# Kernel optimization log

Hardware: AMD Instinct MI355X
Metric: run time of the kernel (lower is better)

The kernel has to match this reference:

```python
import jax, jax.numpy as jnp
import numpy as np

DIM = 1024
NUM_HEADS = 16
HEAD_DIM = DIM // NUM_HEADS
SCALE = HEAD_DIM ** -0.5


def setup_inputs() -> dict:
    key = jax.random.key(0)
    k1, k2, k3 = jax.random.split(key, 3)
    x = jax.random.normal(k1, (4, 2048, DIM), dtype=jnp.float32)
    w_qkv = jax.random.normal(k2, (DIM, 3 * DIM), dtype=jnp.float32) * (DIM ** -0.5)
    b_qkv = jnp.zeros((3 * DIM,), dtype=jnp.float32)
    w_proj = jax.random.normal(k3, (DIM, DIM), dtype=jnp.float32) * (DIM ** -0.5)
    b_proj = jnp.zeros((DIM,), dtype=jnp.float32)
    return {"x": x, "w_qkv": w_qkv, "b_qkv": b_qkv, "w_proj": w_proj, "b_proj": b_proj}


def reference(x, w_qkv, b_qkv, w_proj, b_proj):
    b, n, c = x.shape
    qkv = x @ w_qkv + b_qkv                       # [b, n, 3*dim]
    qkv = qkv.reshape(b, n, 3, NUM_HEADS, HEAD_DIM)
    qkv = jnp.transpose(qkv, (2, 0, 3, 1, 4))     # [3, b, H, n, hd]
    q, k, v = qkv[0], qkv[1], qkv[2]
    attn = jnp.einsum("bhqd,bhkd->bhqk", q, k) * SCALE
    attn = jax.nn.softmax(attn, axis=-1)
    out = jnp.einsum("bhqk,bhkd->bhqd", attn, v)  # [b, H, n, hd]
    out = jnp.transpose(out, (0, 2, 1, 3)).reshape(b, n, c)
    return out @ w_proj + b_proj
```

## Files before the change

### kernel.cpp

```cpp
#include <hip/hip_runtime.h>
#include <hip/hip_bf16.h>

typedef unsigned short u16;
typedef __attribute__((ext_vector_type(8))) short bf16x8;
typedef __attribute__((ext_vector_type(4))) float f32x4;
typedef __attribute__((ext_vector_type(16))) float f32x16;


__device__ __forceinline__ u16 f2bf(float f) {
  union { float f; unsigned u; } v; v.f = f;
  unsigned r = v.u + 0x7fffu + ((v.u >> 16) & 1u);
  return (u16)(r >> 16);
}

#if defined(__has_builtin)
#if __has_builtin(__builtin_amdgcn_cvt_pk_bf16_f32)
#define HAS_PK_BF16 1
#endif
#endif
__device__ __forceinline__ unsigned pk2bf(float a, float b) {
#ifdef HAS_PK_BF16
  typedef __attribute__((ext_vector_type(2))) __bf16 vbf2;
  union { vbf2 v; unsigned u; } u;
  u.v = __builtin_amdgcn_cvt_pk_bf16_f32(a, b);
  return u.u;
#else
  return (unsigned)f2bf(a) | ((unsigned)f2bf(b) << 16);
#endif
}

__device__ __forceinline__ f32x4 mfma16(bf16x8 a, bf16x8 b, f32x4 c) {
  return __builtin_amdgcn_mfma_f32_16x16x32_bf16(a, b, c, 0, 0, 0);
}
__device__ __forceinline__ f32x16 mfma32(bf16x8 a, bf16x8 b, f32x16 c) {
  return __builtin_amdgcn_mfma_f32_32x32x16_bf16(a, b, c, 0, 0, 0);
}

__device__ __forceinline__ void gl_lds16(const void* g, void* l) {
  __builtin_amdgcn_global_load_lds((__attribute__((address_space(1))) void*)g,
                                   (__attribute__((address_space(3))) void*)l,
                                   16, 0, 0);
}

__device__ __forceinline__ void stage128x32(const u16* g0, int ld, u16* lds) {
  const int t = threadIdx.x;
  const int wave = t >> 6;
#pragma unroll
  for (int j = 0; j < 2; ++j) {
    int c = j * 256 + t;
    const u16* gp = g0 + (size_t)(c >> 2) * ld + (c & 3) * 8;
    gl_lds16(gp, lds + (size_t)(j * 256 + wave * 64) * 8);
  }
}


__global__ void cvt_f32_bf16(const float* __restrict__ in, u16* __restrict__ out, int n) {
  int i = (blockIdx.x * blockDim.x + threadIdx.x) * 4;
  if (i >= n) return;
  float4 v = *(const float4*)(in + i);
  u16 o0 = f2bf(v.x), o1 = f2bf(v.y), o2 = f2bf(v.z), o3 = f2bf(v.w);
  ushort4 o; o.x = o0; o.y = o1; o.z = o2; o.w = o3;
  *(ushort4*)(out + i) = o;
}

__global__ void transpose_cvt(const float* __restrict__ in, u16* __restrict__ out,
                              int R, int C) {
  __shared__ u16 tile[64][65];
  int c0 = blockIdx.x * 64, r0 = blockIdx.y * 64;
  int lc = threadIdx.x & 63, lr = threadIdx.x >> 6;
#pragma unroll
  for (int i = 0; i < 16; ++i) {
    int r = lr + i * 4;
    tile[r][lc] = f2bf(in[(size_t)(r0 + r) * C + c0 + lc]);
  }
  __syncthreads();
#pragma unroll
  for (int i = 0; i < 16; ++i) {
    int c = lr + i * 4;
    out[(size_t)(c0 + c) * R + r0 + lc] = tile[lc][c];
  }
}


__global__ __launch_bounds__(256, 2) void gemm_qkv(
    const u16* __restrict__ A, const u16* __restrict__ Bt,
    const float* __restrict__ bias,
    u16* __restrict__ Qb, u16* __restrict__ Kb, u16* __restrict__ Vt) {
  __shared__ u16 smem[128 * 32 * 2];
  u16* As = smem;
  u16* Bs = smem + 4096;
  const int row0 = blockIdx.x * 128, col0 = blockIdx.y * 128;
  const int t = threadIdx.x, lane = t & 63, wave = t >> 6;
  const int quad = lane >> 4, l15 = lane & 15;
  const int m_off = (wave & 1) * 64, n_off = (wave >> 1) * 64;
  f32x4 acc[4][4] = {};
  for (int k0 = 0; k0 < 1024; k0 += 32) {
    __syncthreads();
    stage128x32(A + (size_t)row0 * 1024 + k0, 1024, As);
    stage128x32(Bt + (size_t)col0 * 1024 + k0, 1024, Bs);
    __syncthreads();
    bf16x8 a[4], b[4];
#pragma unroll
    for (int mi = 0; mi < 4; ++mi)
      a[mi] = *(const bf16x8*)(As + (m_off + mi * 16 + l15) * 32 + quad * 8);
#pragma unroll
    for (int ni = 0; ni < 4; ++ni)
      b[ni] = *(const bf16x8*)(Bs + (n_off + ni * 16 + l15) * 32 + quad * 8);
#pragma unroll
    for (int mi = 0; mi < 4; ++mi)
#pragma unroll
      for (int ni = 0; ni < 4; ++ni)
        acc[mi][ni] = mfma16(a[mi], b[ni], acc[mi][ni]);
  }
  const int which = col0 >> 10;

  if (which == 2) {
    u16* Ts = smem;
    const int h0 = (col0 >> 6) & 15;
    const int b_ = row0 >> 11;
    const int s0 = row0 & 2047;
    const int myp = wave >> 1;
#pragma unroll
    for (int p = 0; p < 2; ++p) {
      __syncthreads();
      if (myp == p) {
#pragma unroll
        for (int ni = 0; ni < 4; ++ni) {
          const int d = ni * 16 + l15;
          const float bv = bias[col0 + n_off + ni * 16 + l15];
#pragma unroll
          for (int mi = 0; mi < 4; ++mi) {
            const int sl = m_off + mi * 16 + quad * 4;
            uint2 pk;
            pk.x = pk2bf(acc[mi][ni][0] + bv, acc[mi][ni][1] + bv);
            pk.y = pk2bf(acc[mi][ni][2] + bv, acc[mi][ni][3] + bv);
            *(uint2*)((char*)Ts + d * 256 + ((2 * sl) ^ ((d & 15) << 4))) = pk;
          }
        }
      }
      __syncthreads();
      u16* vt = Vt + ((size_t)(b_ * 16 + h0 + p) * 64) * 2048;
#pragma unroll
      for (int k = 0; k < 4; ++k) {
        int idx = t + 256 * k;
        int d = idx >> 4, c = idx & 15;
        uint4 v = *(const uint4*)((const char*)Ts + d * 256 + ((c ^ (d & 15)) << 4));
        *(uint4*)(vt + (size_t)d * 2048 + s0 + c * 8) = v;
      }
    }
    return;
  }

  u16* dst = which == 0 ? Qb : Kb;
  const float qscale = which == 0 ? 0.1803368801111137f : 1.0f;
#pragma unroll
  for (int ni = 0; ni < 4; ++ni) {
    int col = col0 + n_off + ni * 16 + l15;
    float bv = bias[col];
    int h = (col >> 6) & 15, d = col & 63;
#pragma unroll
    for (int mi = 0; mi < 4; ++mi) {
#pragma unroll
      for (int r = 0; r < 4; ++r) {
        int row = row0 + m_off + mi * 16 + quad * 4 + r;
        int bb = row >> 11, s = row & 2047;
        float v = (acc[mi][ni][r] + bv) * qscale;
        dst[(((size_t)bb * 16 + h) * 2048 + s) * 64 + d] = f2bf(v);
      }
    }
  }
}


__global__ __launch_bounds__(256, 2) void gemm_proj(
    const u16* __restrict__ A, const u16* __restrict__ Bt,
    const float* __restrict__ bias, float* __restrict__ C) {
  __shared__ u16 As[128 * 32], Bs[128 * 32];
  const int row0 = blockIdx.x * 128, col0 = blockIdx.y * 128;
  const int t = threadIdx.x, lane = t & 63, wave = t >> 6;
  const int quad = lane >> 4, l15 = lane & 15;
  const int m_off = (wave & 1) * 64, n_off = (wave >> 1) * 64;
  f32x4 acc[4][4] = {};
  for (int k0 = 0; k0 < 1024; k0 += 32) {
    __syncthreads();
    stage128x32(A + (size_t)row0 * 1024 + k0, 1024, As);
    stage128x32(Bt + (size_t)col0 * 1024 + k0, 1024, Bs);
    __syncthreads();
    bf16x8 a[4], b[4];
#pragma unroll
    for (int mi = 0; mi < 4; ++mi)
      a[mi] = *(const bf16x8*)(As + (m_off + mi * 16 + l15) * 32 + quad * 8);
#pragma unroll
    for (int ni = 0; ni < 4; ++ni)
      b[ni] = *(const bf16x8*)(Bs + (n_off + ni * 16 + l15) * 32 + quad * 8);
#pragma unroll
    for (int mi = 0; mi < 4; ++mi)
#pragma unroll
      for (int ni = 0; ni < 4; ++ni)
        acc[mi][ni] = mfma16(a[mi], b[ni], acc[mi][ni]);
  }
#pragma unroll
  for (int ni = 0; ni < 4; ++ni) {
    int col = col0 + n_off + ni * 16 + l15;
    float bv = bias[col];
#pragma unroll
    for (int mi = 0; mi < 4; ++mi) {
#pragma unroll
      for (int r = 0; r < 4; ++r) {
        int row = row0 + m_off + mi * 16 + quad * 4 + r;
        C[(size_t)row * 1024 + col] = acc[mi][ni][r] + bv;
      }
    }
  }
}


__device__ __forceinline__ void softmax32(const f32x16& s, float& l,
                                          bf16x8& paA, bf16x8& paB) {
  unsigned D[8];
#pragma unroll
  for (int i = 0; i < 8; ++i) {
    float a = __builtin_amdgcn_exp2f(s[2 * i]);
    float b = __builtin_amdgcn_exp2f(s[2 * i + 1]);
    l += a + b;
    D[i] = pk2bf(a, b);
  }
  {
    unsigned x = D[0], x2 = D[1], y = D[2], y2 = D[3];
    asm volatile("v_permlane32_swap_b32 %0, %1" : "+v"(x), "+v"(y));
    asm volatile("v_permlane32_swap_b32 %0, %1" : "+v"(x2), "+v"(y2));
    union { unsigned u[4]; bf16x8 v; } p;
    p.u[0] = x; p.u[1] = x2; p.u[2] = y; p.u[3] = y2;
    paA = p.v;
  }
  {
    unsigned x = D[4], x2 = D[5], y = D[6], y2 = D[7];
    asm volatile("v_permlane32_swap_b32 %0, %1" : "+v"(x), "+v"(y));
    asm volatile("v_permlane32_swap_b32 %0, %1" : "+v"(x2), "+v"(y2));
    union { unsigned u[4]; bf16x8 v; } p;
    p.u[0] = x; p.u[1] = x2; p.u[2] = y; p.u[3] = y2;
    paB = p.v;
  }
}

__global__ __launch_bounds__(256, 2) void attn_kernel(
    const u16* __restrict__ Qb, const u16* __restrict__ Kb,
    const u16* __restrict__ Vt, u16* __restrict__ Ob) {
  __shared__ u16 KsA[64 * 64], KsB[64 * 64];
  __shared__ u16 VsA[64 * 64], VsB[64 * 64];
  const int bh = blockIdx.x, q0 = blockIdx.y * 256;
  const u16* Qp = Qb + (size_t)bh * 2048 * 64;
  const u16* Kp = Kb + (size_t)bh * 2048 * 64;
  const u16* Vp = Vt + (size_t)bh * 64 * 2048;
  const int t = threadIdx.x, lane = t & 63, wave = t >> 6;
  const int l31 = lane & 31, hi = lane >> 5;

  const int kr0 = t >> 3, kc0 = (t & 7) ^ (kr0 & 7);
  const int kr1 = (256 + t) >> 3, kc1 = ((256 + t) & 7) ^ (kr1 & 7);
  const u16* Kg0 = Kp + (size_t)kr0 * 64 + kc0 * 8;
  const u16* Kg1 = Kp + (size_t)kr1 * 64 + kc1 * 8;
  const u16* Vg0 = Vp + (size_t)kr0 * 2048 + kc0 * 8;
  const u16* Vg1 = Vp + (size_t)kr1 * 2048 + kc1 * 8;
  const size_t dof0 = (size_t)wave * 512;
  const size_t dof1 = 2048 + (size_t)wave * 512;

#define STAGE(Kd, Vd, key0)                                   \
  do {                                                        \
    gl_lds16(Kg0 + (size_t)(key0) * 64, (Kd) + dof0);         \
    gl_lds16(Kg1 + (size_t)(key0) * 64, (Kd) + dof1);         \
    gl_lds16(Vg0 + (key0), (Vd) + dof0);                      \
    gl_lds16(Vg1 + (key0), (Vd) + dof1);                      \
  } while (0)

  STAGE(KsA, VsA, 0);
  const u16* Qr0 = Qp + (size_t)(q0 + wave * 64 + l31) * 64 + hi * 8;
  const u16* Qr1 = Qr0 + 32 * 64;
  bf16x8 qf0[4], qf1[4];
#pragma unroll
  for (int dc = 0; dc < 4; ++dc) {
    qf0[dc] = *(const bf16x8*)(Qr0 + dc * 16);
    qf1[dc] = *(const bf16x8*)(Qr1 + dc * 16);
  }
  __syncthreads();

  const int rm = l31 & 7;
  int off[2][4];
#pragma unroll
  for (int x = 0; x < 2; ++x)
#pragma unroll
    for (int c = 0; c < 4; ++c)
      off[x][c] = x * 4096 + l31 * 128 + (((c * 2 + hi) ^ rm) << 4);

  f32x16 acc00 = {}, acc01 = {}, acc10 = {}, acc11 = {};
  float l0 = 0.f, l1 = 0.f;

#define TILE(Ks, Vs)                                                          \
  do {                                                                        \
    _Pragma("unroll")                                                         \
    for (int kh = 0; kh < 2; ++kh) {                                          \
      f32x16 s0 = {}, s1 = {};                                                \
      __builtin_amdgcn_s_setprio(1);                                          \
      _Pragma("unroll")                                                       \
      for (int dc = 0; dc < 4; ++dc) {                                        \
        bf16x8 kf = *(const bf16x8*)((const char*)(Ks) + off[kh][dc]);        \
        s0 = mfma32(kf, qf0[dc], s0);                                         \
        s1 = mfma32(kf, qf1[dc], s1);                                         \
      }                                                                       \
      __builtin_amdgcn_s_setprio(0);                                          \
      bf16x8 pa00, pa01, pa10, pa11;                                          \
      softmax32(s0, l0, pa00, pa01);                                          \
      softmax32(s1, l1, pa10, pa11);                                          \
      __builtin_amdgcn_s_setprio(1);                                          \
      _Pragma("unroll")                                                       \
      for (int ci = 0; ci < 2; ++ci) {                                        \
        const int c = 2 * kh + ci;                                            \
        bf16x8 vlo = *(const bf16x8*)((const char*)(Vs) + off[0][c]);         \
        bf16x8 vhiv = *(const bf16x8*)((const char*)(Vs) + off[1][c]);        \
        bf16x8 pa0 = ci ? pa01 : pa00;                                        \
        bf16x8 pa1 = ci ? pa11 : pa10;                                        \
        acc00 = mfma32(pa0, vlo, acc00);                                      \
        acc01 = mfma32(pa0, vhiv, acc01);                                     \
        acc10 = mfma32(pa1, vlo, acc10);                                      \
        acc11 = mfma32(pa1, vhiv, acc11);                                     \
      }                                                                       \
      __builtin_amdgcn_s_setprio(0);                                          \
    }                                                                         \
  } while (0)

#pragma unroll 1
  for (int kt2 = 0; kt2 < 16; ++kt2) {
    const int kt = kt2 * 2;
    STAGE(KsB, VsB, (kt + 1) * 64);
    TILE(KsA, VsA);
    __syncthreads();
    if (kt2 < 15) STAGE(KsA, VsA, (kt + 2) * 64);
    TILE(KsB, VsB);
    __syncthreads();
  }
#undef TILE
#undef STAGE

  l0 += __shfl_xor(l0, 32);
  l1 += __shfl_xor(l1, 32);
  float inv0 = 1.f / l0, inv1 = 1.f / l1;

  const int b_ = bh >> 4, h = bh & 15;
  const int qw = q0 + wave * 64;
#pragma unroll
  for (int r = 0; r < 16; ++r) {
    const int ql = (r & 3) + 8 * (r >> 2) + 4 * hi;
    float iv0 = __shfl(inv0, ql);
    float iv1 = __shfl(inv1, ql);
    size_t base0 = ((size_t)b_ * 2048 + qw + ql) * 1024 + h * 64;
    size_t base1 = base0 + (size_t)32 * 1024;
    Ob[base0 + l31] = f2bf(acc00[r] * iv0);
    Ob[base0 + 32 + l31] = f2bf(acc01[r] * iv0);
    Ob[base1 + l31] = f2bf(acc10[r] * iv1);
    Ob[base1 + 32 + l31] = f2bf(acc11[r] * iv1);
  }
}


extern "C" void kernel_launch(void* const* d_in, const int* in_sizes, int n_in,
                              void* d_out, int out_size, void* d_ws, size_t ws_size,
                              hipStream_t stream) {
  const float* x      = (const float*)d_in[0];
  const float* w_qkv  = (const float*)d_in[1];
  const float* b_qkv  = (const float*)d_in[2];
  const float* w_proj = (const float*)d_in[3];
  const float* b_proj = (const float*)d_in[4];
  float* out = (float*)d_out;
  char* ws = (char*)d_ws;

  u16* xb    = (u16*)(ws);
  u16* wqkvt = (u16*)(ws + 16777216);
  u16* wprjt = (u16*)(ws + 23068672);
  u16* Qb    = (u16*)(ws + 25165824);
  u16* Kb    = (u16*)(ws + 41943040);
  u16* Vt    = (u16*)(ws + 58720256);
  u16* Ob    = xb;
  if (ws_size < 92274688u) return;

  cvt_f32_bf16<<<8192, 256, 0, stream>>>(x, xb, 8388608);
  transpose_cvt<<<dim3(48, 16), 256, 0, stream>>>(w_qkv, wqkvt, 1024, 3072);
  transpose_cvt<<<dim3(16, 16), 256, 0, stream>>>(w_proj, wprjt, 1024, 1024);
  gemm_qkv<<<dim3(64, 24), 256, 0, stream>>>(xb, wqkvt, b_qkv, Qb, Kb, Vt);
  attn_kernel<<<dim3(64, 8), 256, 0, stream>>>(Qb, Kb, Vt, Ob);
  gemm_proj<<<dim3(64, 8), 256, 0, stream>>>(Ob, wprjt, b_proj, out);
}
```

Baseline: 274.9 us.

## Rewrite QKV and projection GEMMs with 256x256 tiles and double-buffered LDS

Both GEMMs move from 128x128 tiles with 32-wide K steps and two barriers per step to 256x256 tiles, 512 threads, 64-wide K steps, and a double-buffered, swizzled LDS pipeline. Prefetch of the next K slice is interleaved with MFMA groups, using explicit vmcnt waits and s_setprio. The goal is more data reuse per tile, fewer barriers, and memory latency hidden behind compute. The cost is 128KB of LDS per block and fewer blocks: 384 for QKV and only 128 for proj, which may underfill 256 CUs.

New measurement: 270.6 us. About the same (-1.5%).

```diff
diff --git a/kernel.cpp b/kernel.cpp
--- a/kernel.cpp
+++ b/kernel.cpp
@@ -42,17 +42,6 @@
                                    16, 0, 0);
 }
 
-__device__ __forceinline__ void stage128x32(const u16* g0, int ld, u16* lds) {
-  const int t = threadIdx.x;
-  const int wave = t >> 6;
-#pragma unroll
-  for (int j = 0; j < 2; ++j) {
-    int c = j * 256 + t;
-    const u16* gp = g0 + (size_t)(c >> 2) * ld + (c & 3) * 8;
-    gl_lds16(gp, lds + (size_t)(j * 256 + wave * 64) * 8);
-  }
-}
-
 
 __global__ void cvt_f32_bf16(const float* __restrict__ in, u16* __restrict__ out, int n) {
   int i = (blockIdx.x * blockDim.x + threadIdx.x) * 4;
@@ -82,72 +71,136 @@
 }
 
 
-__global__ __launch_bounds__(256, 2) void gemm_qkv(
+struct Smem256 { u16 A0[16384]; u16 B0[16384]; u16 A1[16384]; u16 B1[16384]; };
+
+#define LDB128(base, off) (*(const bf16x8*)((const char*)(base) + (off)))
+#define ISSUE(dst, p, j, k0) \
+  gl_lds16((p) + (size_t)(j) * 65536 + (k0), (dst) + (j) * 4096 + dsel)
+
+#define KSTEP(CA, CB, NA, NB, k0n, PF)                                           \
+  do {                                                                           \
+    bf16x8 aL[4][2], aH[4][2], bL[2][2], bH[2][2];                               \
+        \
+    _Pragma("unroll") for (int mi = 0; mi < 4; ++mi) {                           \
+      aL[mi][0] = LDB128(CA, fA + mi * 2048 + cp0);                              \
+      aL[mi][1] = LDB128(CA, fA + mi * 2048 + cp1);                              \
+    }                                                                            \
+    _Pragma("unroll") for (int ni = 0; ni < 2; ++ni) {                           \
+      bL[ni][0] = LDB128(CB, fB + ni * 2048 + cp0);                              \
+      bL[ni][1] = LDB128(CB, fB + ni * 2048 + cp1);                              \
+    }                                                                            \
+    if (PF) { ISSUE(NB, pB, 0, k0n); ISSUE(NB, pB, 1, k0n); }                    \
+    __builtin_amdgcn_s_setprio(1);                                               \
+    _Pragma("unroll") for (int mi = 0; mi < 4; ++mi)                             \
+      _Pragma("unroll") for (int ni = 0; ni < 2; ++ni) {                         \
+        acc[mi][ni] = mfma16(aL[mi][0], bL[ni][0], acc[mi][ni]);                 \
+        acc[mi][ni] = mfma16(aL[mi][1], bL[ni][1], acc[mi][ni]);                 \
+      }                                                                          \
+    __builtin_amdgcn_s_setprio(0);                                               \
+               \
+    _Pragma("unroll") for (int ni = 0; ni < 2; ++ni) {                           \
+      bH[ni][0] = LDB128(CB, fB + (ni + 2) * 2048 + cp0);                        \
+      bH[ni][1] = LDB128(CB, fB + (ni + 2) * 2048 + cp1);                        \
+    }                                                                            \
+    if (PF) { ISSUE(NB, pB, 2, k0n); ISSUE(NB, pB, 3, k0n); }                    \
+    __builtin_amdgcn_s_setprio(1);                                               \
+    _Pragma("unroll") for (int mi = 0; mi < 4; ++mi)                             \
+      _Pragma("unroll") for (int ni = 0; ni < 2; ++ni) {                         \
+        acc[mi][ni + 2] = mfma16(aL[mi][0], bH[ni][0], acc[mi][ni + 2]);         \
+        acc[mi][ni + 2] = mfma16(aL[mi][1], bH[ni][1], acc[mi][ni + 2]);         \
+      }                                                                          \
+    __builtin_amdgcn_s_setprio(0);                                               \
+            \
+    if (PF) asm volatile("s_waitcnt vmcnt(4)" ::: "memory");                     \
+    else    asm volatile("s_waitcnt vmcnt(0)" ::: "memory");                     \
+    __builtin_amdgcn_s_barrier();                                                \
+    _Pragma("unroll") for (int mi = 0; mi < 4; ++mi) {                           \
+      aH[mi][0] = LDB128(CA, fA + (mi + 4) * 2048 + cp0);                        \
+      aH[mi][1] = LDB128(CA, fA + (mi + 4) * 2048 + cp1);                        \
+    }                                                                            \
+    if (PF) { ISSUE(NA, pA, 0, k0n); ISSUE(NA, pA, 2, k0n); }                    \
+    __builtin_amdgcn_s_setprio(1);                                               \
+    _Pragma("unroll") for (int mi = 0; mi < 4; ++mi)                             \
+      _Pragma("unroll") for (int ni = 0; ni < 2; ++ni) {                         \
+        acc[mi + 4][ni + 2] = mfma16(aH[mi][0], bH[ni][0], acc[mi + 4][ni + 2]); \
+        acc[mi + 4][ni + 2] = mfma16(aH[mi][1], bH[ni][1], acc[mi + 4][ni + 2]); \
+      }                                                                          \
+    __builtin_amdgcn_s_setprio(0);                                               \
+              \
+    if (PF) { ISSUE(NA, pA, 1, k0n); ISSUE(NA, pA, 3, k0n); }                    \
+    __builtin_amdgcn_s_setprio(1);                                               \
+    _Pragma("unroll") for (int mi = 0; mi < 4; ++mi)                             \
+      _Pragma("unroll") for (int ni = 0; ni < 2; ++ni) {                         \
+        acc[mi + 4][ni] = mfma16(aH[mi][0], bL[ni][0], acc[mi + 4][ni]);         \
+        acc[mi + 4][ni] = mfma16(aH[mi][1], bL[ni][1], acc[mi + 4][ni]);         \
+      }                                                                          \
+    __builtin_amdgcn_s_setprio(0);                                               \
+    if (PF) asm volatile("s_waitcnt vmcnt(2)" ::: "memory");                     \
+    __builtin_amdgcn_s_barrier();                                                \
+  } while (0)
+
+#define GEMM256_SETUP(Amat, Bmat)                                                \
+  __shared__ Smem256 sm;                                                         \
+  const int t = threadIdx.x, lane = t & 63, wave = t >> 6;                       \
+  const int quad = lane >> 4, l15 = lane & 15;                                   \
+  const int wm = wave >> 2, wn = wave & 3;                                       \
+  const int row0 = blockIdx.x * 256, col0 = blockIdx.y * 256;                    \
+  const int rowb = t >> 3, lc = (t & 7) ^ ((t >> 3) & 7);                        \
+  const u16* pA = (Amat) + (size_t)(row0 + rowb) * 1024 + lc * 8;                \
+  const u16* pB = (Bmat) + (size_t)(col0 + rowb) * 1024 + lc * 8;                \
+  const size_t dsel = (size_t)wave * 512;                                        \
+  const int fA = (wm * 128 + l15) * 128;                                         \
+  const int fB = (wn * 64 + l15) * 128;                                          \
+  const int cp0 = ((quad) ^ (l15 & 7)) << 4;                                     \
+  const int cp1 = ((quad + 4) ^ (l15 & 7)) << 4;                                 \
+  f32x4 acc[8][4] = {};                                                          \
+  ISSUE(sm.B0, pB, 0, 0); ISSUE(sm.B0, pB, 1, 0);                                \
+  ISSUE(sm.B0, pB, 2, 0); ISSUE(sm.B0, pB, 3, 0);                                \
+  ISSUE(sm.A0, pA, 0, 0); ISSUE(sm.A0, pA, 2, 0);                                \
+  ISSUE(sm.A0, pA, 1, 0); ISSUE(sm.A0, pA, 3, 0);                                \
+  asm volatile("s_waitcnt vmcnt(2)" ::: "memory");                               \
+  __builtin_amdgcn_s_barrier();                                                  \
+  _Pragma("unroll 1")                                                            \
+  for (int kk = 0; kk < 8; ++kk) {                                               \
+    const int k0 = kk * 128;                                                     \
+    KSTEP(sm.A0, sm.B0, sm.A1, sm.B1, k0 + 64, 1);                               \
+    KSTEP(sm.A1, sm.B1, sm.A0, sm.B0, k0 + 128, (kk < 7));                       \
+  }
+
+
+__global__ __launch_bounds__(512, 2) void gemm_qkv(
     const u16* __restrict__ A, const u16* __restrict__ Bt,
     const float* __restrict__ bias,
     u16* __restrict__ Qb, u16* __restrict__ Kb, u16* __restrict__ Vt) {
-  __shared__ u16 smem[128 * 32 * 2];
-  u16* As = smem;
-  u16* Bs = smem + 4096;
-  const int row0 = blockIdx.x * 128, col0 = blockIdx.y * 128;
-  const int t = threadIdx.x, lane = t & 63, wave = t >> 6;
-  const int quad = lane >> 4, l15 = lane & 15;
-  const int m_off = (wave & 1) * 64, n_off = (wave >> 1) * 64;
-  f32x4 acc[4][4] = {};
-  for (int k0 = 0; k0 < 1024; k0 += 32) {
-    __syncthreads();
-    stage128x32(A + (size_t)row0 * 1024 + k0, 1024, As);
-    stage128x32(Bt + (size_t)col0 * 1024 + k0, 1024, Bs);
-    __syncthreads();
-    bf16x8 a[4], b[4];
-#pragma unroll
-    for (int mi = 0; mi < 4; ++mi)
-      a[mi] = *(const bf16x8*)(As + (m_off + mi * 16 + l15) * 32 + quad * 8);
-#pragma unroll
-    for (int ni = 0; ni < 4; ++ni)
-      b[ni] = *(const bf16x8*)(Bs + (n_off + ni * 16 + l15) * 32 + quad * 8);
-#pragma unroll
-    for (int mi = 0; mi < 4; ++mi)
-#pragma unroll
-      for (int ni = 0; ni < 4; ++ni)
-        acc[mi][ni] = mfma16(a[mi], b[ni], acc[mi][ni]);
-  }
+  GEMM256_SETUP(A, Bt)
+
   const int which = col0 >> 10;
 
   if (which == 2) {
-    u16* Ts = smem;
-    const int h0 = (col0 >> 6) & 15;
-    const int b_ = row0 >> 11;
-    const int s0 = row0 & 2047;
-    const int myp = wave >> 1;
-#pragma unroll
-    for (int p = 0; p < 2; ++p) {
-      __syncthreads();
-      if (myp == p) {
-#pragma unroll
-        for (int ni = 0; ni < 4; ++ni) {
-          const int d = ni * 16 + l15;
-          const float bv = bias[col0 + n_off + ni * 16 + l15];
-#pragma unroll
-          for (int mi = 0; mi < 4; ++mi) {
-            const int sl = m_off + mi * 16 + quad * 4;
-            uint2 pk;
-            pk.x = pk2bf(acc[mi][ni][0] + bv, acc[mi][ni][1] + bv);
-            pk.y = pk2bf(acc[mi][ni][2] + bv, acc[mi][ni][3] + bv);
-            *(uint2*)((char*)Ts + d * 256 + ((2 * sl) ^ ((d & 15) << 4))) = pk;
-          }
-        }
-      }
-      __syncthreads();
-      u16* vt = Vt + ((size_t)(b_ * 16 + h0 + p) * 64) * 2048;
-#pragma unroll
-      for (int k = 0; k < 4; ++k) {
-        int idx = t + 256 * k;
-        int d = idx >> 4, c = idx & 15;
-        uint4 v = *(const uint4*)((const char*)Ts + d * 256 + ((c ^ (d & 15)) << 4));
-        *(uint4*)(vt + (size_t)d * 2048 + s0 + c * 8) = v;
+    u16* Ts = ((u16*)&sm) + wave * 8192;
+#pragma unroll
+    for (int ni = 0; ni < 4; ++ni) {
+      const int d = ni * 16 + l15;
+      const float bv = bias[col0 + wn * 64 + ni * 16 + l15];
+#pragma unroll
+      for (int mi = 0; mi < 8; ++mi) {
+        const int s = mi * 16 + quad * 4;
+        uint2 pk;
+        pk.x = pk2bf(acc[mi][ni][0] + bv, acc[mi][ni][1] + bv);
+        pk.y = pk2bf(acc[mi][ni][2] + bv, acc[mi][ni][3] + bv);
+        *(uint2*)((char*)Ts + d * 256 + (((s >> 3) ^ (d & 15)) << 4) + (s & 4) * 2) = pk;
       }
     }
+    const int h = ((col0 - 2048) >> 6) + wn;
+    const int b_ = row0 >> 11;
+    const int s0w = (row0 & 2047) + wm * 128;
+    u16* vt = Vt + ((size_t)(b_ * 16 + h) * 64) * 2048;
+#pragma unroll
+    for (int it = 0; it < 16; ++it) {
+      const int d = it * 4 + quad;
+      uint4 v = *(const uint4*)((const char*)Ts + d * 256 + ((l15 ^ (d & 15)) << 4));
+      *(uint4*)(vt + (size_t)d * 2048 + s0w + l15 * 8) = v;
+    }
     return;
   }
 
@@ -155,59 +208,37 @@
   const float qscale = which == 0 ? 0.1803368801111137f : 1.0f;
 #pragma unroll
   for (int ni = 0; ni < 4; ++ni) {
-    int col = col0 + n_off + ni * 16 + l15;
-    float bv = bias[col];
-    int h = (col >> 6) & 15, d = col & 63;
-#pragma unroll
-    for (int mi = 0; mi < 4; ++mi) {
+    const int col = (col0 & 1023) + wn * 64 + ni * 16 + l15;
+    const float bv = bias[col0 + wn * 64 + ni * 16 + l15];
+    const int h = col >> 6, d = col & 63;
+#pragma unroll
+    for (int mi = 0; mi < 8; ++mi) {
 #pragma unroll
       for (int r = 0; r < 4; ++r) {
-        int row = row0 + m_off + mi * 16 + quad * 4 + r;
-        int bb = row >> 11, s = row & 2047;
-        float v = (acc[mi][ni][r] + bv) * qscale;
-        dst[(((size_t)bb * 16 + h) * 2048 + s) * 64 + d] = f2bf(v);
+        const int row = row0 + wm * 128 + mi * 16 + quad * 4 + r;
+        const int bb = row >> 11, s = row & 2047;
+        dst[(((size_t)bb * 16 + h) * 2048 + s) * 64 + d] =
+            f2bf((acc[mi][ni][r] + bv) * qscale);
       }
     }
   }
 }
 
 
-__global__ __launch_bounds__(256, 2) void gemm_proj(
+__global__ __launch_bounds__(512, 2) void gemm_proj(
     const u16* __restrict__ A, const u16* __restrict__ Bt,
     const float* __restrict__ bias, float* __restrict__ C) {
-  __shared__ u16 As[128 * 32], Bs[128 * 32];
-  const int row0 = blockIdx.x * 128, col0 = blockIdx.y * 128;
-  const int t = threadIdx.x, lane = t & 63, wave = t >> 6;
-  const int quad = lane >> 4, l15 = lane & 15;
-  const int m_off = (wave & 1) * 64, n_off = (wave >> 1) * 64;
-  f32x4 acc[4][4] = {};
-  for (int k0 = 0; k0 < 1024; k0 += 32) {
-    __syncthreads();
-    stage128x32(A + (size_t)row0 * 1024 + k0, 1024, As);
-    stage128x32(Bt + (size_t)col0 * 1024 + k0, 1024, Bs);
-    __syncthreads();
-    bf16x8 a[4], b[4];
-#pragma unroll
-    for (int mi = 0; mi < 4; ++mi)
-      a[mi] = *(const bf16x8*)(As + (m_off + mi * 16 + l15) * 32 + quad * 8);
-#pragma unroll
-    for (int ni = 0; ni < 4; ++ni)
-      b[ni] = *(const bf16x8*)(Bs + (n_off + ni * 16 + l15) * 32 + quad * 8);
-#pragma unroll
-    for (int mi = 0; mi < 4; ++mi)
-#pragma unroll
-      for (int ni = 0; ni < 4; ++ni)
-        acc[mi][ni] = mfma16(a[mi], b[ni], acc[mi][ni]);
-  }
+  GEMM256_SETUP(A, Bt)
+
 #pragma unroll
   for (int ni = 0; ni < 4; ++ni) {
-    int col = col0 + n_off + ni * 16 + l15;
-    float bv = bias[col];
-#pragma unroll
-    for (int mi = 0; mi < 4; ++mi) {
+    const int col = col0 + wn * 64 + ni * 16 + l15;
+    const float bv = bias[col];
+#pragma unroll
+    for (int mi = 0; mi < 8; ++mi) {
 #pragma unroll
       for (int r = 0; r < 4; ++r) {
-        int row = row0 + m_off + mi * 16 + quad * 4 + r;
+        const int row = row0 + wm * 128 + mi * 16 + quad * 4 + r;
         C[(size_t)row * 1024 + col] = acc[mi][ni][r] + bv;
       }
     }
@@ -384,7 +415,7 @@
   cvt_f32_bf16<<<8192, 256, 0, stream>>>(x, xb, 8388608);
   transpose_cvt<<<dim3(48, 16), 256, 0, stream>>>(w_qkv, wqkvt, 1024, 3072);
   transpose_cvt<<<dim3(16, 16), 256, 0, stream>>>(w_proj, wprjt, 1024, 1024);
-  gemm_qkv<<<dim3(64, 24), 256, 0, stream>>>(xb, wqkvt, b_qkv, Qb, Kb, Vt);
+  gemm_qkv<<<dim3(32, 12), 512, 0, stream>>>(xb, wqkvt, b_qkv, Qb, Kb, Vt);
   attn_kernel<<<dim3(64, 8), 256, 0, stream>>>(Qb, Kb, Vt, Ob);
-  gemm_proj<<<dim3(64, 8), 256, 0, stream>>>(Ob, wprjt, b_proj, out);
-}
+  gemm_proj<<<dim3(32, 4), 512, 0, stream>>>(Ob, wprjt, b_proj, out);
+}
```
